# Performance work log

Hardware: AMD Instinct MI355X
Metric: run time of the kernel (lower is better)

## Reference

```python
import jax, jax.numpy as jnp
import numpy as np

N_SPH = 7
N_RAD = 6
CUTOFF = 5.0
P = 5  # envelope exponent
E = 500000
T = 2000000

# ---- numpy-side precompute of spherical Bessel roots & normalizers ----
# matches sympy bessel_basis(n,k): basis[l][j] = N_{l,j} * j_l(z_{l,j} * x)

def _sph_jn_np(t, l):
    t = np.asarray(t, dtype=np.float64)
    j0 = np.sin(t) / t
    if l == 0:
        return j0
    j1 = np.sin(t) / t**2 - np.cos(t) / t
    for i in range(2, l + 1):
        j0, j1 = j1, (2 * i - 1) / t * j1 - j0
    return j1


def _jn_zeros(n, k):
    # k-th zeros of spherical bessel j_l for l=0..n-1, via interlacing + bisection
    nz = k + n - 1
    zeros = np.zeros((n, nz))
    zeros[0] = np.arange(1, nz + 1) * np.pi  # zeros of j_0
    for l in range(1, n):
        for i in range(nz - l):
            a, b = zeros[l - 1, i], zeros[l - 1, i + 1]
            fa = _sph_jn_np(a, l)
            for _ in range(80):
                m = 0.5 * (a + b)
                fm = _sph_jn_np(m, l)
                if fa * fm <= 0:
                    b = m
                else:
                    a, fa = m, fm
            zeros[l, i] = 0.5 * (a + b)
    return zeros[:, :k]

_Z = _jn_zeros(N_SPH, N_RAD)  # [n, k]
_NORM = np.sqrt(2.0) / np.abs(np.stack([_sph_jn_np(_Z[l], l + 1) for l in range(N_SPH)]))
FREQ = jnp.asarray(_Z, dtype=jnp.float32)   # [n, k]
NORM = jnp.asarray(_NORM, dtype=jnp.float32)  # [n, k]
# real sph harm (m=0): Y_l(theta) = sqrt((2l+1)/4pi) * P_l(cos theta)
Y_COEF = jnp.asarray(np.sqrt((2 * np.arange(N_SPH) + 1) / (4 * np.pi)), dtype=jnp.float32)


def _sph_jn(t, l):
    j0 = jnp.sin(t) / t
    if l == 0:
        return j0
    j1 = jnp.sin(t) / t**2 - jnp.cos(t) / t
    for i in range(2, l + 1):
        j0, j1 = j1, (2 * i - 1) / t * j1 - j0
    return j1


def _forward(dist, angle, idx_kj):
    n, k = N_SPH, N_RAD
    x = dist / CUTOFF  # [E]
    # radial basis: [E, n*k], layout l-major / j-minor like torch stack order
    rbf = jnp.concatenate(
        [NORM[l] * _sph_jn(x[:, None] * FREQ[l], l) for l in range(n)], axis=1)
    # envelope (DimeNet variant: no cutoff masking)
    a = -(P + 1) * (P + 2) / 2.0
    b = float(P * (P + 2))
    c = -P * (P + 1) / 2.0
    xp = x**P
    env = 1.0 / x + a * xp + b * xp * x + c * xp * x * x
    rbf = env[:, None] * rbf
    # angular basis via Legendre recurrence on cos(theta)
    cth = jnp.cos(angle)
    Ps = [jnp.ones_like(cth), cth]
    for l in range(2, n):
        Ps.append(((2 * l - 1) * cth * Ps[-1] - (l - 1) * Ps[-2]) / l)
    cbf = jnp.stack([Y_COEF[l] * Ps[l] for l in range(n)], axis=1)  # [T, n]
    out = (rbf[idx_kj].reshape(-1, n, k) * cbf[:, :, None]).reshape(-1, n * k)
    return out


def setup_inputs() -> dict:
    key = jax.random.key(0)
    k1, k2, k3 = jax.random.split(key, 3)
    # distances kept away from 0 (envelope has 1/x term)
    dist = jax.random.uniform(k1, (E,), jnp.float32, 0.1, 1.0) * CUTOFF
    angle = jax.random.uniform(k2, (T,), jnp.float32, 0.0, float(np.pi))
    idx_kj = jax.random.randint(k3, (T,), 0, E)
    return {"dist": dist, "angle": angle, "idx_kj": idx_kj}


def reference(dist, angle, idx_kj):
    return _forward(dist, angle, idx_kj)
```

## Files before the change

kernel.cpp:

```cpp
#include <hip/hip_runtime.h>
#include <hip/hip_bf16.h>
#include <cmath>

#define N_SPH 7
#define N_RAD 6
#define NC (N_SPH * N_RAD)
#define INV_CUTOFF 0.2f

typedef float f2 __attribute__((ext_vector_type(2)));
typedef float f4 __attribute__((ext_vector_type(4)));

struct BesselConsts {
    float freq[NC];
    float norm[NC];
    float ycoef[N_SPH];
};

static double h_sph_jn(double t, int l) {
    double j0 = sin(t) / t;
    if (l == 0) return j0;
    double j1 = sin(t) / (t * t) - cos(t) / t;
    for (int i = 2; i <= l; i++) {
        double j2 = (2.0 * i - 1.0) / t * j1 - j0;
        j0 = j1; j1 = j2;
    }
    return j1;
}

static void compute_consts(BesselConsts* bc) {
    const int n = N_SPH, k = N_RAD, nz = N_RAD + N_SPH - 1;
    const double PI = 3.14159265358979323846;
    double zeros[N_SPH][12];
    for (int i = 0; i < nz; i++) zeros[0][i] = (i + 1) * PI;
    for (int l = 1; l < n; l++) {
        for (int i = 0; i < nz - l; i++) {
            double a = zeros[l - 1][i], b = zeros[l - 1][i + 1];
            double fa = h_sph_jn(a, l);
            for (int it = 0; it < 80; it++) {
                double m = 0.5 * (a + b);
                double fm = h_sph_jn(m, l);
                if (fa * fm <= 0.0) { b = m; } else { a = m; fa = fm; }
            }
            zeros[l][i] = 0.5 * (a + b);
        }
    }
    for (int l = 0; l < n; l++)
        for (int j = 0; j < k; j++) {
            bc->freq[l * k + j] = (float)zeros[l][j];
            bc->norm[l * k + j] =
                (float)(sqrt(2.0) / fabs(h_sph_jn(zeros[l][j], l + 1)));
        }
    for (int l = 0; l < n; l++)
        bc->ycoef[l] = (float)sqrt((2.0 * l + 1.0) / (4.0 * PI));
}

__global__ __launch_bounds__(256) void fused_row_kernel(
    const float* __restrict__ dist, const float* __restrict__ angle,
    const int* __restrict__ idx, float* __restrict__ out, int T_,
    BesselConsts bc) {
    __shared__ __align__(16) float stage[256 * NC];
    const int tix = threadIdx.x;
    const int t0 = blockIdx.x * 256;
    const int t = t0 + tix;
    const bool valid = t < T_;

    float x = 0.5f, cth = 0.0f;
    if (valid) {
        x = dist[idx[t]] * INV_CUTOFF;
        cth = cosf(angle[t]);
    }
    float xp = x * x * x * x * x;
    float env = 1.0f / x + xp * (-21.0f + x * (35.0f - 15.0f * x));
    float P[N_SPH];
    P[0] = 1.0f;
    P[1] = cth;
#pragma unroll
    for (int l = 2; l < N_SPH; ++l)
        P[l] = ((2 * l - 1) * cth * P[l - 1] - (l - 1) * P[l - 2]) *
               (1.0f / (float)l);
    float yP[N_SPH];
#pragma unroll
    for (int l = 0; l < N_SPH; ++l) yP[l] = bc.ycoef[l] * P[l];

#pragma unroll
    for (int l = 0; l < N_SPH; ++l) {
#pragma unroll
        for (int j = 0; j < N_RAD; ++j) {
            const int c = l * N_RAD + j;
            float tt = x * bc.freq[c];
            float s, co;
            sincosf(tt, &s, &co);
            float rf = 1.0f / tt;
            double r = (double)rf;
            r = r * (2.0 - (double)tt * r);
            double jv;
            double j0 = (double)s * r;
            if (l == 0) {
                jv = j0;
            } else {
                double j1 = ((double)s * r - (double)co) * r;
#pragma unroll
                for (int i = 2; i <= l; ++i) {
                    double j2 = (2.0 * i - 1.0) * r * j1 - j0;
                    j0 = j1; j1 = j2;
                }
                jv = j1;
            }
            stage[tix * NC + c] = yP[l] * (env * bc.norm[c] * (float)jv);
        }
    }
    __syncthreads();

    const int rows = min(256, T_ - t0);
    const int nelem = rows * NC;
    const int n4 = nelem >> 2;
    const size_t base = (size_t)t0 * NC;
#pragma unroll
    for (int it = 0; it < 11; ++it) {
        int i = it * 256 + tix;
        if (i < n4) {
            f4 v = *reinterpret_cast<const f4*>(&stage[4 * i]);
            __builtin_nontemporal_store(
                v, reinterpret_cast<f4*>(out + base + 4 * (size_t)i));
        }
    }
    for (int i = n4 * 4 + tix; i < nelem; i += 256)
        __builtin_nontemporal_store(stage[i], out + base + i);
}

extern "C" void kernel_launch(void* const* d_in, const int* in_sizes, int n_in,
                              void* d_out, int out_size, void* d_ws,
                              size_t ws_size, hipStream_t stream) {
    const float* dist = (const float*)d_in[0];
    const float* angle = (const float*)d_in[1];
    const int* idx = (const int*)d_in[2];
    float* out = (float*)d_out;

    int E_ = in_sizes[0];
    int T_ = in_sizes[1];
    (void)E_; (void)d_ws; (void)ws_size;

    BesselConsts bc;
    compute_consts(&bc);

    fused_row_kernel<<<(T_ + 255) / 256, 256, 0, stream>>>(dist, angle, idx,
                                                           out, T_, bc);
}
```

Measured before the change: 418.2 us.

## Replace per-element sincos with angle-addition from shared multiples of pi/2

Each argument x*freq is split as x*(m*pi/2) + x*delta. The sin/cos of x*m*pi/2 come from one double-precision Taylor evaluation stepped by angle addition, and a short polynomial covers the small residual. Low orders (l<=3) move to FP32 recurrences, while l>=4 keep FP64 to limit cancellation error. This removes 42 full sincosf calls and much FP64 work per row, at the cost of a serial double-precision rotation chain and possible accuracy loss.

```diff
diff --git a/kernel.cpp b/kernel.cpp
--- a/kernel.cpp
+++ b/kernel.cpp
@@ -10,10 +10,21 @@
 typedef float f2 __attribute__((ext_vector_type(2)));
 typedef float f4 __attribute__((ext_vector_type(4)));
 
+static constexpr int M_TAB[NC] = {
+    2,  4,  6,  8,  10, 12,
+    3,  5,  7,  9,  11, 13,
+    4,  6,  8,  10, 12, 14,
+    4,  7,  9,  11, 13, 15,
+    5,  7,  10, 12, 14, 16,
+    6,  8,  10, 13, 15, 17,
+    7,  9,  11, 13, 15, 18};
+
 struct BesselConsts {
     float freq[NC];
     float norm[NC];
+    float deltaf[NC];
     float ycoef[N_SPH];
+    double deltad[NC];
 };
 
 static double h_sph_jn(double t, int l) {
@@ -30,6 +41,7 @@
 static void compute_consts(BesselConsts* bc) {
     const int n = N_SPH, k = N_RAD, nz = N_RAD + N_SPH - 1;
     const double PI = 3.14159265358979323846;
+    const double PI_2 = 1.57079632679489661923;
     double zeros[N_SPH][12];
     for (int i = 0; i < nz; i++) zeros[0][i] = (i + 1) * PI;
     for (int l = 1; l < n; l++) {
@@ -46,12 +58,78 @@
     }
     for (int l = 0; l < n; l++)
         for (int j = 0; j < k; j++) {
-            bc->freq[l * k + j] = (float)zeros[l][j];
-            bc->norm[l * k + j] =
+            const int c = l * k + j;
+            bc->freq[c] = (float)zeros[l][j];
+            bc->norm[c] =
                 (float)(sqrt(2.0) / fabs(h_sph_jn(zeros[l][j], l + 1)));
+            double dd = zeros[l][j] - (double)M_TAB[c] * PI_2;
+            bc->deltad[c] = dd;
+            bc->deltaf[c] = (float)dd;
         }
     for (int l = 0; l < n; l++)
         bc->ycoef[l] = (float)sqrt((2.0 * l + 1.0) / (4.0 * PI));
+}
+
+template <int L, int C_>
+__device__ __forceinline__ void elem32(float x, float env, float Sf, float Cf,
+                                       const float* yP, float* strow,
+                                       const BesselConsts& bc) {
+    float tt = x * bc.freq[C_];
+    float u = x * bc.deltaf[C_];
+    float v = u * u;
+    float su = u * fmaf(v, fmaf(v, fmaf(v, fmaf(v, fmaf(v, -2.5052108e-8f,
+                    2.7557319e-6f), -1.9841270e-4f), 8.3333333e-3f),
+                    -1.6666667e-1f), 1.0f);
+    float cu = fmaf(v, fmaf(v, fmaf(v, fmaf(v, fmaf(v, fmaf(v, 2.0876757e-9f,
+                    -2.7557319e-7f), 2.4801587e-5f), -1.3888889e-3f),
+                    4.1666667e-2f), -0.5f), 1.0f);
+    float s = fmaf(Sf, cu, Cf * su);
+    float co = fmaf(Cf, cu, -(Sf * su));
+    float r = __builtin_amdgcn_rcpf(tt);
+    r = r * fmaf(-tt, r, 2.0f);
+    float jv;
+    float j0 = s * r;
+    if constexpr (L == 0) {
+        jv = j0;
+    } else {
+        float j1 = fmaf(s, r, -co) * r;
+#pragma unroll
+        for (int i = 2; i <= L; ++i) {
+            float j2 = fmaf((2.0f * i - 1.0f) * r, j1, -j0);
+            j0 = j1; j1 = j2;
+        }
+        jv = j1;
+    }
+    strow[C_] = yP[L] * (env * bc.norm[C_] * jv);
+}
+
+template <int L, int C_>
+__device__ __forceinline__ void elem64(float x, double xd, float env,
+                                       double Sd, double Cd, const float* yP,
+                                       float* strow, const BesselConsts& bc) {
+    float tt = x * bc.freq[C_];
+    double u = xd * bc.deltad[C_];
+    double v = u * u;
+    double su = u * fma(v, fma(v, fma(v, fma(v, fma(v, -1.0 / 39916800.0,
+                     1.0 / 362880.0), -1.0 / 5040.0), 1.0 / 120.0),
+                     -1.0 / 6.0), 1.0);
+    double cu = fma(v, fma(v, fma(v, fma(v, fma(v, fma(v, 1.0 / 479001600.0,
+                     -1.0 / 3628800.0), 1.0 / 40320.0), -1.0 / 720.0),
+                     1.0 / 24.0), -0.5), 1.0);
+    double s = fma(Sd, cu, Cd * su);
+    double co = fma(Cd, cu, -(Sd * su));
+    double td = (double)tt;
+    float rf = __builtin_amdgcn_rcpf(tt);
+    double r = (double)rf;
+    r = r * fma(-td, r, 2.0);
+    double j0 = s * r;
+    double j1 = fma(s, r, -co) * r;
+#pragma unroll
+    for (int i = 2; i <= L; ++i) {
+        double j2 = fma((2.0 * i - 1.0) * r, j1, -j0);
+        j0 = j1; j1 = j2;
+    }
+    strow[C_] = yP[L] * (env * bc.norm[C_] * (float)j1);
 }
 
 __global__ __launch_bounds__(256) void fused_row_kernel(
@@ -82,33 +160,47 @@
 #pragma unroll
     for (int l = 0; l < N_SPH; ++l) yP[l] = bc.ycoef[l] * P[l];
 
-#pragma unroll
-    for (int l = 0; l < N_SPH; ++l) {
-#pragma unroll
-        for (int j = 0; j < N_RAD; ++j) {
-            const int c = l * N_RAD + j;
-            float tt = x * bc.freq[c];
-            float s, co;
-            sincosf(tt, &s, &co);
-            float rf = 1.0f / tt;
-            double r = (double)rf;
-            r = r * (2.0 - (double)tt * r);
-            double jv;
-            double j0 = (double)s * r;
-            if (l == 0) {
-                jv = j0;
-            } else {
-                double j1 = ((double)s * r - (double)co) * r;
-#pragma unroll
-                for (int i = 2; i <= l; ++i) {
-                    double j2 = (2.0 * i - 1.0) * r * j1 - j0;
-                    j0 = j1; j1 = j2;
-                }
-                jv = j1;
-            }
-            stage[tix * NC + c] = yP[l] * (env * bc.norm[c] * (float)jv);
-        }
-    }
+    double xd = (double)x;
+    double th = xd * 1.57079632679489661923;
+    double w = th * th;
+    double s1 = th * fma(w, fma(w, fma(w, fma(w, fma(w, fma(w,
+                     1.0 / 6227020800.0, -1.0 / 39916800.0), 1.0 / 362880.0),
+                     -1.0 / 5040.0), 1.0 / 120.0), -1.0 / 6.0), 1.0);
+    double c1 = fma(w, fma(w, fma(w, fma(w, fma(w, fma(w, fma(w,
+                     -1.0 / 87178291200.0, 1.0 / 479001600.0),
+                     -1.0 / 3628800.0), 1.0 / 40320.0), -1.0 / 720.0),
+                     1.0 / 24.0), -0.5), 1.0);
+    double S = s1, C = c1;
+
+    float* strow = &stage[tix * NC];
+
+#define STEP() do { double Sn = fma(S, c1, C * s1); \
+                    C = fma(C, c1, -(S * s1)); S = Sn; } while (0)
+#define E32(L_, C_) do { float Sf = (float)S, Cf = (float)C; \
+                         elem32<L_, C_>(x, env, Sf, Cf, yP, strow, bc); } while (0)
+#define E64(L_, C_) elem64<L_, C_>(x, xd, env, S, C, yP, strow, bc)
+
+    STEP();  E32(0, 0);
+    STEP();  E32(1, 6);
+    STEP();  E32(0, 1);  E32(2, 12); E32(3, 18);
+    STEP();  E32(1, 7);  E64(4, 24);
+    STEP();  E32(0, 2);  E32(2, 13); E64(5, 30);
+    STEP();  E32(1, 8);  E32(3, 19); E64(4, 25); E64(6, 36);
+    STEP();  E32(0, 3);  E32(2, 14); E64(5, 31);
+    STEP();  E32(1, 9);  E32(3, 20); E64(6, 37);
+    STEP();  E32(0, 4);  E32(2, 15); E64(4, 26); E64(5, 32);
+    STEP();  E32(1, 10); E32(3, 21); E64(6, 38);
+    STEP();  E32(0, 5);  E32(2, 16); E64(4, 27);
+    STEP();  E32(1, 11); E32(3, 22); E64(5, 33); E64(6, 39);
+    STEP();  E32(2, 17); E64(4, 28);
+    STEP();  E32(3, 23); E64(5, 34); E64(6, 40);
+    STEP();  E64(4, 29);
+    STEP();  E64(5, 35);
+    STEP();  E64(6, 41);
+#undef STEP
+#undef E32
+#undef E64
+
     __syncthreads();
 
     const int rows = min(256, T_ - t0);
```

Measured after the change: 374.2 us. -10.5%, faster.
